# Kernel tuning notes

Hardware: AMD Instinct MI355X
Metric: run time of the kernel (lower is better)

Reference implementation:

```python
import jax, jax.numpy as jnp
import numpy as np

N_NODES = 50000
N_EDGES = 800000
IN_DIM = 128
HID_DIM = 128
N_CLASSES = 32
X_STEPS = 2
BN_EPS = 1e-5


def _agg(h, src, dst):
    # PyG 'add' aggregation with self-loops: out[i] = sum_{(j->i) in E} h[j] + h[i]
    return jax.ops.segment_sum(h[src], dst, num_segments=h.shape[0]) + h


def setup_inputs() -> dict:
    key = jax.random.key(0)
    ks = jax.random.split(key, 8)
    x = jax.random.normal(ks[0], (N_NODES, IN_DIM), dtype=jnp.float32)
    edge_index = jax.random.randint(ks[1], (2, N_EDGES), 0, N_NODES, dtype=jnp.int64)
    s1 = 1.0 / np.sqrt(IN_DIM)
    W1 = jax.random.uniform(ks[2], (IN_DIM, HID_DIM), jnp.float32, -s1, s1)
    b1 = jax.random.uniform(ks[3], (HID_DIM,), jnp.float32, -s1, s1)
    gamma = jnp.ones((HID_DIM,), jnp.float32)
    beta = jnp.zeros((HID_DIM,), jnp.float32)
    s2 = 1.0 / np.sqrt(HID_DIM)
    W2 = jax.random.uniform(ks[4], (HID_DIM, N_CLASSES), jnp.float32, -s2, s2)
    b2 = jax.random.uniform(ks[5], (N_CLASSES,), jnp.float32, -s2, s2)
    return {"x": x, "edge_index": edge_index, "W1": W1, "b1": b1,
            "gamma": gamma, "beta": beta, "W2": W2, "b2": b2}


def reference(x, edge_index, W1, b1, gamma, beta, W2, b2):
    src, dst = edge_index[0], edge_index[1]
    # conv1: K-step sum aggregation, then Linear
    h = x
    for _ in range(X_STEPS):
        h = _agg(h, src, dst)
    h = h @ W1 + b1
    # BatchNorm (training mode: batch statistics over nodes)
    mu = jnp.mean(h, axis=0)
    var = jnp.mean(jnp.square(h - mu), axis=0)  # biased variance, as torch BN uses
    h = (h - mu) * jax.lax.rsqrt(var + BN_EPS) * gamma + beta
    h = jax.nn.selu(h)
    # dropout p=0.0 -> identity
    # conv2: 1-step aggregation + Linear
    h = _agg(h, src, dst)
    h = h @ W2 + b2
    return jax.nn.softmax(h, axis=1)
```

## Files before the change

### kernel.cpp

```cpp
#include <hip/hip_runtime.h>

#define NN 50000
#define NE 800000
#define DIM 128
#define NC 32
#define CB 782
#define CCH 13
#define EB 8192
#define NBLK 98
#define BN_EPS 1e-5f
#define SELU_ALPHA 1.6732632423543772f
#define SELU_SCALE 1.0507009873554805f

typedef __attribute__((ext_vector_type(8))) short bf16x8;
typedef __attribute__((ext_vector_type(4))) float f32x4;

#define FMA16(acc, hv, w0, w1, w2, w3)                                   \
    acc.x = fmaf(hv.x, w0.x, acc.x); acc.y = fmaf(hv.x, w0.y, acc.y);    \
    acc.z = fmaf(hv.x, w0.z, acc.z); acc.w = fmaf(hv.x, w0.w, acc.w);    \
    acc.x = fmaf(hv.y, w1.x, acc.x); acc.y = fmaf(hv.y, w1.y, acc.y);    \
    acc.z = fmaf(hv.y, w1.z, acc.z); acc.w = fmaf(hv.y, w1.w, acc.w);    \
    acc.x = fmaf(hv.z, w2.x, acc.x); acc.y = fmaf(hv.z, w2.y, acc.y);    \
    acc.z = fmaf(hv.z, w2.z, acc.z); acc.w = fmaf(hv.z, w2.w, acc.w);    \
    acc.x = fmaf(hv.w, w3.x, acc.x); acc.y = fmaf(hv.w, w3.y, acc.y);    \
    acc.z = fmaf(hv.w, w3.z, acc.z); acc.w = fmaf(hv.w, w3.w, acc.w);

#define BNSELU1(v)                                                        \
    v = v > 0.f ? SELU_SCALE * v : SELU_SCALE * SELU_ALPHA * (__expf(v) - 1.f);
#define BNSELU4(hv, sc, sh)                                               \
    hv.x = fmaf(hv.x, sc.x, sh.x); BNSELU1(hv.x)                          \
    hv.y = fmaf(hv.y, sc.y, sh.y); BNSELU1(hv.y)                          \
    hv.z = fmaf(hv.z, sc.z, sh.z); BNSELU1(hv.z)                          \
    hv.w = fmaf(hv.w, sc.w, sh.w); BNSELU1(hv.w)

__device__ __forceinline__ float bf_lo(unsigned u) { return __uint_as_float(u << 16); }
__device__ __forceinline__ float bf_hi(unsigned u) { return __uint_as_float(u & 0xffff0000u); }
__device__ __forceinline__ unsigned bf_round(float a) {
    unsigned ba = __float_as_uint(a);
    return (ba + 0x7fffu + ((ba >> 16) & 1u)) >> 16;
}
__device__ __forceinline__ unsigned pack_bf16(float a, float b) {
    return bf_round(a) | (bf_round(b) << 16);
}

__global__ void k_detect(const int* __restrict__ raw, int* __restrict__ flag) {
    int v = raw[2 * threadIdx.x + 1];
    unsigned long long b = __ballot(v == 0);
    if (threadIdx.x == 0) *flag = (b == 0xFFFFFFFFFFFFFFFFULL) ? 1 : 0;
}

__global__ void k_zero_f(float* __restrict__ p, int n) {
    int i = blockIdx.x * blockDim.x + threadIdx.x;
    if (i < n) p[i] = 0.f;
}

__global__ void k_cvt(const float4* __restrict__ in, uint2* __restrict__ out, int n4) {
    int i = blockIdx.x * blockDim.x + threadIdx.x;
    if (i < n4) {
        float4 v = in[i];
        out[i] = make_uint2(pack_bf16(v.x, v.y), pack_bf16(v.z, v.w));
    }
}

__global__ void k_cvtw(const float* __restrict__ W1, ushort* __restrict__ w1t) {
    int i = blockIdx.x * 256 + threadIdx.x;
    if (i < DIM * DIM) {
        int k = i >> 7, n = i & 127;
        w1t[n * 136 + k] = (ushort)bf_round(W1[i]);
    }
}

__global__ __launch_bounds__(256) void k_bcount(const void* __restrict__ raw,
                                                const int* __restrict__ flag,
                                                int* __restrict__ cnt) {
    __shared__ int lh[CB];
    int blk = blockIdx.x, tid = threadIdx.x;
    for (int t = tid; t < CB; t += 256) lh[t] = 0;
    __syncthreads();
    int f = *flag;
    const long long* r64 = (const long long*)raw;
    const int* r32 = (const int*)raw;
    int e0 = blk * EB;
    int n = min(EB, NE - e0);
    for (int i = tid; i < n; i += 256) {
        int d = f ? (int)r64[NE + e0 + i] : r32[NE + e0 + i];
        atomicAdd(&lh[d >> 6], 1);
    }
    __syncthreads();
    for (int t = tid; t < CB; t += 256) cnt[t * NBLK + blk] = lh[t];
}

__global__ void k_colscan(int* __restrict__ cnt, int* __restrict__ tot) {
    int b = blockIdx.x;
    int* row = cnt + b * NBLK;
    int l = threadIdx.x;
    int p0 = 2 * l, p1 = 2 * l + 1;
    int a0 = (p0 < NBLK) ? row[p0] : 0;
    int a1 = (p1 < NBLK) ? row[p1] : 0;
    int s = a0 + a1, inc = s;
    #pragma unroll
    for (int off = 1; off < 64; off <<= 1) {
        int u = __shfl_up(inc, off, 64);
        if (l >= off) inc += u;
    }
    int ex = inc - s;
    if (p0 < NBLK) row[p0] = ex;
    if (p1 < NBLK) row[p1] = ex + a0;
    if (l == 63) tot[b] = inc;
}

__global__ void k_cscan(const int* __restrict__ tot, int* __restrict__ cbase,
                        int* __restrict__ rowptr) {
    int lane = threadIdx.x;
    int base = lane * CCH;
    int loc[CCH];
    int s = 0;
    #pragma unroll
    for (int i = 0; i < CCH; ++i) {
        int idx = base + i;
        int v = (idx < CB) ? tot[idx] : 0;
        loc[i] = s; s += v;
    }
    int inc = s;
    #pragma unroll
    for (int off = 1; off < 64; off <<= 1) {
        int u = __shfl_up(inc, off, 64);
        if (lane >= off) inc += u;
    }
    int ex = inc - s;
    #pragma unroll
    for (int i = 0; i < CCH; ++i) {
        int idx = base + i;
        if (idx < CB) cbase[idx] = ex + loc[i];
    }
    if (lane == 63) { cbase[CB] = inc; rowptr[NN] = NE; }
}

__global__ __launch_bounds__(256) void k_cscatter2(const void* __restrict__ raw,
                                                   const int* __restrict__ flag,
                                                   const int* __restrict__ cnt,
                                                   const int* __restrict__ cbase,
                                                   unsigned* __restrict__ pairs) {
    __shared__ int lh[CB], lbase[CB], lcur[CB], gbase[CB];
    __shared__ unsigned lp[EB];
    int blk = blockIdx.x, tid = threadIdx.x;
    for (int t = tid; t < CB; t += 256) {
        lh[t] = 0;
        gbase[t] = cbase[t] + cnt[t * NBLK + blk];
    }
    __syncthreads();
    int f = *flag;
    const long long* r64 = (const long long*)raw;
    const int* r32 = (const int*)raw;
    int e0 = blk * EB;
    int n = min(EB, NE - e0);
    for (int i = tid; i < n; i += 256) {
        int d = f ? (int)r64[NE + e0 + i] : r32[NE + e0 + i];
        atomicAdd(&lh[d >> 6], 1);
    }
    __syncthreads();
    if (tid < 64) {
        int base = tid * CCH;
        int loc[CCH];
        int s = 0;
        #pragma unroll
        for (int i = 0; i < CCH; ++i) {
            int idx = base + i;
            int v = (idx < CB) ? lh[idx] : 0;
            loc[i] = s; s += v;
        }
        int inc = s;
        #pragma unroll
        for (int off = 1; off < 64; off <<= 1) {
            int u = __shfl_up(inc, off, 64);
            if (tid >= off) inc += u;
        }
        int ex = inc - s;
        #pragma unroll
        for (int i = 0; i < CCH; ++i) {
            int idx = base + i;
            if (idx < CB) lbase[idx] = ex + loc[i];
        }
    }
    __syncthreads();
    for (int t = tid; t < CB; t += 256) lcur[t] = lbase[t];
    __syncthreads();
    for (int i = tid; i < n; i += 256) {
        int d = f ? (int)r64[NE + e0 + i] : r32[NE + e0 + i];
        int sv = f ? (int)r64[e0 + i] : r32[e0 + i];
        int b = d >> 6;
        int p = atomicAdd(&lcur[b], 1);
        lp[p] = (unsigned)sv | ((unsigned)(d & 63) << 16) | ((unsigned)b << 22);
    }
    __syncthreads();
    for (int i = tid; i < n; i += 256) {
        unsigned pr = lp[i];
        int b = pr >> 22;
        pairs[gbase[b] + (i - lbase[b])] = pr;
    }
}

__global__ __launch_bounds__(256) void k_bucket(const unsigned* __restrict__ pairs,
                                                const int* __restrict__ cbase,
                                                int* __restrict__ rowptr,
                                                int* __restrict__ eidx) {
    __shared__ int cnt[64], cur[64];
    int b = blockIdx.x;
    int tid = threadIdx.x;
    if (tid < 64) cnt[tid] = 0;
    __syncthreads();
    int lo = cbase[b], hi = cbase[b + 1];
    for (int i = lo + tid; i < hi; i += 256)
        atomicAdd(&cnt[(pairs[i] >> 16) & 63], 1);
    __syncthreads();
    if (tid < 64) {
        int v = cnt[tid];
        int inc = v;
        #pragma unroll
        for (int off = 1; off < 64; off <<= 1) {
            int u = __shfl_up(inc, off, 64);
            if (tid >= off) inc += u;
        }
        int ex = inc - v;
        cur[tid] = ex;
        int node = b * 64 + tid;
        if (node < NN) rowptr[node] = lo + ex;
    }
    __syncthreads();
    for (int i = lo + tid; i < hi; i += 256) {
        unsigned pr = pairs[i];
        int p = atomicAdd(&cur[(pr >> 16) & 63], 1);
        eidx[lo + p] = (int)(pr & 0xFFFFu);
    }
}

__global__ __launch_bounds__(256) void k_gather_bf(const unsigned* __restrict__ in,
                                                   unsigned* __restrict__ out,
                                                   const int* __restrict__ rowptr,
                                                   const int* __restrict__ eidx) {
    int node = blockIdx.x * 4 + (threadIdx.x >> 6);
    if (node >= NN) return;
    int lane = threadIdx.x & 63;
    unsigned su = in[(size_t)node * 64 + lane];
    float2 acc = {bf_lo(su), bf_hi(su)};
    int b = rowptr[node], e = rowptr[node + 1];
    int j = b;
    for (; j + 3 < e; j += 4) {
        int s0 = eidx[j], s1 = eidx[j + 1], s2 = eidx[j + 2], s3 = eidx[j + 3];
        unsigned u0 = in[(size_t)s0 * 64 + lane];
        unsigned u1 = in[(size_t)s1 * 64 + lane];
        unsigned u2 = in[(size_t)s2 * 64 + lane];
        unsigned u3 = in[(size_t)s3 * 64 + lane];
        acc.x += bf_lo(u0) + bf_lo(u1) + bf_lo(u2) + bf_lo(u3);
        acc.y += bf_hi(u0) + bf_hi(u1) + bf_hi(u2) + bf_hi(u3);
    }
    for (; j < e; ++j) {
        unsigned u0 = in[(size_t)eidx[j] * 64 + lane];
        acc.x += bf_lo(u0);
        acc.y += bf_hi(u0);
    }
    out[(size_t)node * 64 + lane] = pack_bf16(acc.x, acc.y);
}

__global__ __launch_bounds__(256) void k_gemm1(
    const unsigned* __restrict__ hBb, const ushort* __restrict__ w1t,
    const float* __restrict__ b1, float* __restrict__ h1,
    float* __restrict__ ssum, float* __restrict__ ssq) {
    __shared__ __align__(16) ushort wT[DIM * 136];
    __shared__ float redS[4 * DIM];
    __shared__ float redQ[4 * DIM];
    int tid = threadIdx.x;
    for (int i = tid; i < DIM * 136 / 8; i += 256)
        ((uint4*)wT)[i] = ((const uint4*)w1t)[i];
    for (int i = tid; i < 4 * DIM; i += 256) { redS[i] = 0.f; redQ[i] = 0.f; }
    __syncthreads();

    int wid = tid >> 6, lane = tid & 63;
    int cl = lane & 15, kg = lane >> 4;
    int tile = blockIdx.x * 4 + wid;
    if (tile < NN / 16) {
        int rbase = tile * 16;
        const uint4* arow = (const uint4*)(hBb + (size_t)(rbase + cl) * 64);
        f32x4 acc[8];
        #pragma unroll
        for (int ct = 0; ct < 8; ++ct) acc[ct] = (f32x4){0.f, 0.f, 0.f, 0.f};
        #pragma unroll
        for (int kk = 0; kk < 4; ++kk) {
            union { uint4 u; bf16x8 f; } a;
            a.u = arow[kk * 4 + kg];
            #pragma unroll
            for (int ct = 0; ct < 8; ++ct) {
                union { uint4 u; bf16x8 f; } bb;
                bb.u = *(const uint4*)&wT[(ct * 16 + cl) * 136 + kk * 32 + kg * 8];
                acc[ct] = __builtin_amdgcn_mfma_f32_16x16x32_bf16(a.f, bb.f, acc[ct], 0, 0, 0);
            }
        }
        #pragma unroll
        for (int ct = 0; ct < 8; ++ct) {
            int col = ct * 16 + cl;
            float bias = b1[col];
            float s = 0.f, q = 0.f;
            #pragma unroll
            for (int i = 0; i < 4; ++i) {
                float v = acc[ct][i] + bias;
                h1[(size_t)(rbase + kg * 4 + i) * DIM + col] = v;
                s += v; q += v * v;
            }
            s += __shfl_xor(s, 16); s += __shfl_xor(s, 32);
            q += __shfl_xor(q, 16); q += __shfl_xor(q, 32);
            if (kg == 0) { redS[wid * DIM + col] = s; redQ[wid * DIM + col] = q; }
        }
    }
    __syncthreads();
    if (tid < DIM) {
        float S = redS[tid] + redS[DIM + tid] + redS[2 * DIM + tid] + redS[3 * DIM + tid];
        float Q = redQ[tid] + redQ[DIM + tid] + redQ[2 * DIM + tid] + redQ[3 * DIM + tid];
        atomicAdd(&ssum[tid], S);
        atomicAdd(&ssq[tid], Q);
    }
}

__global__ void k_bnstats(const float* __restrict__ ssum, const float* __restrict__ ssq,
                          const float* __restrict__ gamma, const float* __restrict__ beta,
                          float* __restrict__ scale, float* __restrict__ shift) {
    int c = threadIdx.x;
    float mu = ssum[c] / (float)NN;
    float var = ssq[c] / (float)NN - mu * mu;
    float rs = rsqrtf(var + BN_EPS);
    float sc = rs * gamma[c];
    scale[c] = sc;
    shift[c] = beta[c] - mu * sc;
}

__global__ __launch_bounds__(256) void k_gemm2(const float* __restrict__ h,
                                               const float* __restrict__ W2,
                                               const float* __restrict__ scale,
                                               const float* __restrict__ shift,
                                               unsigned* __restrict__ tb) {
    __shared__ float w[DIM * NC];
    __shared__ float scl[DIM], shl[DIM];
    for (int i = threadIdx.x * 4; i < DIM * NC; i += 1024)
        *(float4*)&w[i] = *(const float4*)&W2[i];
    if (threadIdx.x < DIM) {
        scl[threadIdx.x] = scale[threadIdx.x];
        shl[threadIdx.x] = shift[threadIdx.x];
    }
    __syncthreads();

    int c0 = (threadIdx.x & 7) * 4;
    int rg = threadIdx.x >> 3;
    int r0 = blockIdx.x * 128 + rg * 4;
    if (r0 >= NN) return;
    const float* h0 = h + (size_t)r0 * DIM;
    float4 a0 = {0, 0, 0, 0}, a1 = {0, 0, 0, 0}, a2 = {0, 0, 0, 0}, a3 = {0, 0, 0, 0};
    #pragma unroll 4
    for (int k4 = 0; k4 < DIM / 4; ++k4) {
        float4 sc = *(const float4*)&scl[k4 * 4];
        float4 sh = *(const float4*)&shl[k4 * 4];
        float4 hv0 = *(const float4*)&h0[k4 * 4];
        float4 hv1 = *(const float4*)&h0[DIM + k4 * 4];
        float4 hv2 = *(const float4*)&h0[2 * DIM + k4 * 4];
        float4 hv3 = *(const float4*)&h0[3 * DIM + k4 * 4];
        BNSELU4(hv0, sc, sh)
        BNSELU4(hv1, sc, sh)
        BNSELU4(hv2, sc, sh)
        BNSELU4(hv3, sc, sh)
        float4 w0 = *(const float4*)&w[(k4 * 4 + 0) * NC + c0];
        float4 w1 = *(const float4*)&w[(k4 * 4 + 1) * NC + c0];
        float4 w2 = *(const float4*)&w[(k4 * 4 + 2) * NC + c0];
        float4 w3 = *(const float4*)&w[(k4 * 4 + 3) * NC + c0];
        FMA16(a0, hv0, w0, w1, w2, w3)
        FMA16(a1, hv1, w0, w1, w2, w3)
        FMA16(a2, hv2, w0, w1, w2, w3)
        FMA16(a3, hv3, w0, w1, w2, w3)
    }
    ((uint2*)tb)[((size_t)r0 * 16 + c0 / 2) / 2]       = make_uint2(pack_bf16(a0.x, a0.y), pack_bf16(a0.z, a0.w));
    ((uint2*)tb)[((size_t)(r0 + 1) * 16 + c0 / 2) / 2] = make_uint2(pack_bf16(a1.x, a1.y), pack_bf16(a1.z, a1.w));
    ((uint2*)tb)[((size_t)(r0 + 2) * 16 + c0 / 2) / 2] = make_uint2(pack_bf16(a2.x, a2.y), pack_bf16(a2.z, a2.w));
    ((uint2*)tb)[((size_t)(r0 + 3) * 16 + c0 / 2) / 2] = make_uint2(pack_bf16(a3.x, a3.y), pack_bf16(a3.z, a3.w));
}

__global__ __launch_bounds__(256) void k_gsoftmax(const unsigned* __restrict__ tb,
                                                  const float* __restrict__ b2,
                                                  const int* __restrict__ rowptr,
                                                  const int* __restrict__ eidx,
                                                  float* __restrict__ out) {
    int node = blockIdx.x * 4 + (threadIdx.x >> 6);
    if (node >= NN) return;
    int lane = threadIdx.x & 63;
    int c2 = lane & 15;
    int g = lane >> 4;
    float2 acc = {0.f, 0.f};
    if (g == 0) {
        unsigned u = tb[(size_t)node * 16 + c2];
        acc.x = bf_lo(u); acc.y = bf_hi(u);
    }
    int b = rowptr[node], e = rowptr[node + 1];
    for (int j = b + g; j < e; j += 4) {
        unsigned u = tb[(size_t)eidx[j] * 16 + c2];
        acc.x += bf_lo(u);
        acc.y += bf_hi(u);
    }
    acc.x += __shfl_xor(acc.x, 16); acc.x += __shfl_xor(acc.x, 32);
    acc.y += __shfl_xor(acc.y, 16); acc.y += __shfl_xor(acc.y, 32);
    acc.x += b2[2 * c2];
    acc.y += b2[2 * c2 + 1];
    float m = fmaxf(acc.x, acc.y);
    #pragma unroll
    for (int off = 8; off; off >>= 1) m = fmaxf(m, __shfl_xor(m, off, 16));
    float2 ex = {__expf(acc.x - m), __expf(acc.y - m)};
    float s = ex.x + ex.y;
    #pragma unroll
    for (int off = 8; off; off >>= 1) s += __shfl_xor(s, off, 16);
    float inv = 1.f / s;
    if (g == 0)
        *(float2*)&out[(size_t)node * NC + 2 * c2] = make_float2(ex.x * inv, ex.y * inv);
}

extern "C" void kernel_launch(void* const* d_in, const int* in_sizes, int n_in,
                              void* d_out, int out_size, void* d_ws, size_t ws_size,
                              hipStream_t stream) {
    const float* x     = (const float*)d_in[0];
    const void*  eraw  = d_in[1];
    const float* W1    = (const float*)d_in[2];
    const float* b1    = (const float*)d_in[3];
    const float* gamma = (const float*)d_in[4];
    const float* beta  = (const float*)d_in[5];
    const float* W2    = (const float*)d_in[6];
    const float* b2    = (const float*)d_in[7];
    float* out = (float*)d_out;

    float*    regA = (float*)d_ws;
    unsigned* xb   = (unsigned*)regA;
    unsigned* hAb  = xb + (size_t)NN * 64;
    float*    h1   = regA;
    float*    regB = regA + (size_t)NN * DIM;
    unsigned* pairs= (unsigned*)regB;
    unsigned* hBb  = (unsigned*)regB;
    unsigned* tb   = (unsigned*)(regB + (size_t)NN * 64);
    int* eidx   = (int*)(regB + (size_t)NN * DIM);
    int* rowptr = eidx + NE;
    int* cnt    = rowptr + NN + 4;
    int* tot    = cnt + CB * NBLK;
    int* cbase  = tot + 784;
    float* ssum  = (float*)(cbase + 784);
    float* ssq   = ssum + DIM;
    float* scale = ssq + DIM;
    float* shift = scale + DIM;
    ushort* w1t  = (ushort*)(shift + DIM);
    int*   flag  = (int*)((char*)w1t + DIM * 136 * sizeof(ushort));

    const int n4 = NN * DIM / 4;

    k_detect<<<1, 64, 0, stream>>>((const int*)eraw, flag);
    k_zero_f<<<1, 256, 0, stream>>>(ssum, 2 * DIM);
    k_bcount<<<NBLK, 256, 0, stream>>>(eraw, flag, cnt);
    k_colscan<<<CB, 64, 0, stream>>>(cnt, tot);
    k_cscan<<<1, 64, 0, stream>>>(tot, cbase, rowptr);
    k_cscatter2<<<NBLK, 256, 0, stream>>>(eraw, flag, cnt, cbase, pairs);
    k_bucket<<<CB, 256, 0, stream>>>(pairs, cbase, rowptr, eidx);

    k_cvt<<<(n4 + 255) / 256, 256, 0, stream>>>((const float4*)x, (uint2*)xb, n4);
    k_cvtw<<<(DIM * DIM + 255) / 256, 256, 0, stream>>>(W1, w1t);

    const int gather_blocks = (NN + 3) / 4;
    k_gather_bf<<<gather_blocks, 256, 0, stream>>>(xb, hAb, rowptr, eidx);
    k_gather_bf<<<gather_blocks, 256, 0, stream>>>(hAb, hBb, rowptr, eidx);
    k_gemm1<<<(NN / 16 + 3) / 4, 256, 0, stream>>>(hBb, w1t, b1, h1, ssum, ssq);
    k_bnstats<<<1, DIM, 0, stream>>>(ssum, ssq, gamma, beta, scale, shift);
    k_gemm2<<<(NN + 127) / 128, 256, 0, stream>>>(h1, W2, scale, shift, tb);
    k_gsoftmax<<<gather_blocks, 256, 0, stream>>>(tb, b2, rowptr, eidx, out);
}
```

Baseline: 224.5 us.

## Split bf16 gathers into feature-quarter passes and merge small prep kernels

Each 128-wide bf16 gather now runs as four launches. Each launch covers a 32-feature quarter (64 bytes per row), and the four 16-lane groups of a wave walk different neighbours before a shuffle reduction. The aim is a smaller per-pass working set that stays in L2/MALL, so random row gathers hit cache more often. Index loads and output stores become nontemporal, and the detect/zero and x/W1 conversion kernels are fused to cut launches. The cost is reading rowptr/eidx four times per step, six extra launches, and partly used 64-byte row segments.

```diff
diff --git a/kernel.cpp b/kernel.cpp
--- a/kernel.cpp
+++ b/kernel.cpp
@@ -14,6 +14,7 @@
 
 typedef __attribute__((ext_vector_type(8))) short bf16x8;
 typedef __attribute__((ext_vector_type(4))) float f32x4;
+typedef __attribute__((ext_vector_type(2))) float f32x2;
 
 #define FMA16(acc, hv, w0, w1, w2, w3)                                   \
     acc.x = fmaf(hv.x, w0.x, acc.x); acc.y = fmaf(hv.x, w0.y, acc.y);    \
@@ -43,30 +44,32 @@
     return bf_round(a) | (bf_round(b) << 16);
 }
 
-__global__ void k_detect(const int* __restrict__ raw, int* __restrict__ flag) {
-    int v = raw[2 * threadIdx.x + 1];
-    unsigned long long b = __ballot(v == 0);
-    if (threadIdx.x == 0) *flag = (b == 0xFFFFFFFFFFFFFFFFULL) ? 1 : 0;
-}
-
-__global__ void k_zero_f(float* __restrict__ p, int n) {
-    int i = blockIdx.x * blockDim.x + threadIdx.x;
-    if (i < n) p[i] = 0.f;
-}
-
-__global__ void k_cvt(const float4* __restrict__ in, uint2* __restrict__ out, int n4) {
-    int i = blockIdx.x * blockDim.x + threadIdx.x;
-    if (i < n4) {
+__global__ void k_detect(const int* __restrict__ raw, int* __restrict__ flag,
+                         float* __restrict__ z) {
+    if (blockIdx.x == 0) {
+        if (threadIdx.x < 64) {
+            int v = raw[2 * threadIdx.x + 1];
+            unsigned long long b = __ballot(v == 0);
+            if (threadIdx.x == 0) *flag = (b == 0xFFFFFFFFFFFFFFFFULL) ? 1 : 0;
+        }
+    } else {
+        z[threadIdx.x] = 0.f;
+    }
+}
+
+#define CVT_BLOCKS 6250
+__global__ void k_prep(const float4* __restrict__ in, uint2* __restrict__ out,
+                       const float* __restrict__ W1, ushort* __restrict__ w1t) {
+    if (blockIdx.x < CVT_BLOCKS) {
+        int i = blockIdx.x * 256 + threadIdx.x;
         float4 v = in[i];
         out[i] = make_uint2(pack_bf16(v.x, v.y), pack_bf16(v.z, v.w));
-    }
-}
-
-__global__ void k_cvtw(const float* __restrict__ W1, ushort* __restrict__ w1t) {
-    int i = blockIdx.x * 256 + threadIdx.x;
-    if (i < DIM * DIM) {
-        int k = i >> 7, n = i & 127;
-        w1t[n * 136 + k] = (ushort)bf_round(W1[i]);
+    } else {
+        int i = (blockIdx.x - CVT_BLOCKS) * 256 + threadIdx.x;
+        if (i < DIM * DIM) {
+            int k = i >> 7, n = i & 127;
+            w1t[n * 136 + k] = (ushort)bf_round(W1[i]);
+        }
     }
 }
 
@@ -234,32 +237,43 @@
     }
 }
 
-__global__ __launch_bounds__(256) void k_gather_bf(const unsigned* __restrict__ in,
-                                                   unsigned* __restrict__ out,
-                                                   const int* __restrict__ rowptr,
-                                                   const int* __restrict__ eidx) {
+__global__ __launch_bounds__(256) void k_gather_q(const unsigned* __restrict__ in,
+                                                  unsigned* __restrict__ out,
+                                                  const int* __restrict__ rowptr,
+                                                  const int* __restrict__ eidx,
+                                                  int q) {
     int node = blockIdx.x * 4 + (threadIdx.x >> 6);
     if (node >= NN) return;
     int lane = threadIdx.x & 63;
-    unsigned su = in[(size_t)node * 64 + lane];
-    float2 acc = {bf_lo(su), bf_hi(su)};
+    int c = lane & 15;
+    int g = lane >> 4;
+    int off = q * 16 + c;
+    float2 acc = {0.f, 0.f};
+    if (g == 0) {
+        unsigned su = in[(size_t)node * 64 + off];
+        acc.x = bf_lo(su); acc.y = bf_hi(su);
+    }
     int b = rowptr[node], e = rowptr[node + 1];
-    int j = b;
-    for (; j + 3 < e; j += 4) {
-        int s0 = eidx[j], s1 = eidx[j + 1], s2 = eidx[j + 2], s3 = eidx[j + 3];
-        unsigned u0 = in[(size_t)s0 * 64 + lane];
-        unsigned u1 = in[(size_t)s1 * 64 + lane];
-        unsigned u2 = in[(size_t)s2 * 64 + lane];
-        unsigned u3 = in[(size_t)s3 * 64 + lane];
-        acc.x += bf_lo(u0) + bf_lo(u1) + bf_lo(u2) + bf_lo(u3);
-        acc.y += bf_hi(u0) + bf_hi(u1) + bf_hi(u2) + bf_hi(u3);
-    }
-    for (; j < e; ++j) {
-        unsigned u0 = in[(size_t)eidx[j] * 64 + lane];
+    int j = b + g;
+    for (; j + 4 < e; j += 8) {
+        int s0 = __builtin_nontemporal_load(&eidx[j]);
+        int s1 = __builtin_nontemporal_load(&eidx[j + 4]);
+        unsigned u0 = in[(size_t)s0 * 64 + off];
+        unsigned u1 = in[(size_t)s1 * 64 + off];
+        acc.x += bf_lo(u0) + bf_lo(u1);
+        acc.y += bf_hi(u0) + bf_hi(u1);
+    }
+    if (j < e) {
+        int s0 = __builtin_nontemporal_load(&eidx[j]);
+        unsigned u0 = in[(size_t)s0 * 64 + off];
         acc.x += bf_lo(u0);
         acc.y += bf_hi(u0);
     }
-    out[(size_t)node * 64 + lane] = pack_bf16(acc.x, acc.y);
+    acc.x += __shfl_xor(acc.x, 16); acc.x += __shfl_xor(acc.x, 32);
+    acc.y += __shfl_xor(acc.y, 16); acc.y += __shfl_xor(acc.y, 32);
+    if (g == 0)
+        __builtin_nontemporal_store(pack_bf16(acc.x, acc.y),
+                                    &out[(size_t)node * 64 + off]);
 }
 
 __global__ __launch_bounds__(256) void k_gemm1(
@@ -397,7 +411,8 @@
     }
     int b = rowptr[node], e = rowptr[node + 1];
     for (int j = b + g; j < e; j += 4) {
-        unsigned u = tb[(size_t)eidx[j] * 16 + c2];
+        int s = __builtin_nontemporal_load(&eidx[j]);
+        unsigned u = tb[(size_t)s * 16 + c2];
         acc.x += bf_lo(u);
         acc.y += bf_hi(u);
     }
@@ -413,8 +428,10 @@
     #pragma unroll
     for (int off = 8; off; off >>= 1) s += __shfl_xor(s, off, 16);
     float inv = 1.f / s;
-    if (g == 0)
-        *(float2*)&out[(size_t)node * NC + 2 * c2] = make_float2(ex.x * inv, ex.y * inv);
+    if (g == 0) {
+        f32x2 r = {ex.x * inv, ex.y * inv};
+        __builtin_nontemporal_store(r, (f32x2*)&out[(size_t)node * NC + 2 * c2]);
+    }
 }
 
 extern "C" void kernel_launch(void* const* d_in, const int* in_sizes, int n_in,
@@ -450,22 +467,20 @@
     ushort* w1t  = (ushort*)(shift + DIM);
     int*   flag  = (int*)((char*)w1t + DIM * 136 * sizeof(ushort));
 
-    const int n4 = NN * DIM / 4;
-
-    k_detect<<<1, 64, 0, stream>>>((const int*)eraw, flag);
-    k_zero_f<<<1, 256, 0, stream>>>(ssum, 2 * DIM);
+    k_detect<<<2, 256, 0, stream>>>((const int*)eraw, flag, ssum);
     k_bcount<<<NBLK, 256, 0, stream>>>(eraw, flag, cnt);
     k_colscan<<<CB, 64, 0, stream>>>(cnt, tot);
     k_cscan<<<1, 64, 0, stream>>>(tot, cbase, rowptr);
     k_cscatter2<<<NBLK, 256, 0, stream>>>(eraw, flag, cnt, cbase, pairs);
     k_bucket<<<CB, 256, 0, stream>>>(pairs, cbase, rowptr, eidx);
 
-    k_cvt<<<(n4 + 255) / 256, 256, 0, stream>>>((const float4*)x, (uint2*)xb, n4);
-    k_cvtw<<<(DIM * DIM + 255) / 256, 256, 0, stream>>>(W1, w1t);
+    k_prep<<<CVT_BLOCKS + 64, 256, 0, stream>>>((const float4*)x, (uint2*)xb, W1, w1t);
 
     const int gather_blocks = (NN + 3) / 4;
-    k_gather_bf<<<gather_blocks, 256, 0, stream>>>(xb, hAb, rowptr, eidx);
-    k_gather_bf<<<gather_blocks, 256, 0, stream>>>(hAb, hBb, rowptr, eidx);
+    for (int q = 0; q < 4; ++q)
+        k_gather_q<<<gather_blocks, 256, 0, stream>>>(xb, hAb, rowptr, eidx, q);
+    for (int q = 0; q < 4; ++q)
+        k_gather_q<<<gather_blocks, 256, 0, stream>>>(hAb, hBb, rowptr, eidx, q);
     k_gemm1<<<(NN / 16 + 3) / 4, 256, 0, stream>>>(hBb, w1t, b1, h1, ssum, ssq);
     k_bnstats<<<1, DIM, 0, stream>>>(ssum, ssq, gamma, beta, scale, shift);
     k_gemm2<<<(NN + 127) / 128, 256, 0, stream>>>(h1, W2, scale, shift, tb);
```

After: 370.4 us. 65.0% more time.
